# Optimization experiments

Hardware: AMD Instinct MI355X
Metric: run time of the kernel (lower is better)

The kernel has to match this reference:

```python
import jax, jax.numpy as jnp
import numpy as np

WS = 16                     # window_size
OW = 24                     # overlap_win_size = int(16*0.5)+16
PAD = (OW - WS) // 2        # unfold padding = 4
DIM = 384
HEADS = 6
HID = 768                   # mlp_ratio 2.0 * dim
TABLE = (WS + OW - 1) ** 2  # 1521


def _rel_pos_index():
    ch = np.arange(WS)
    coords = np.stack(np.meshgrid(ch, ch, indexing='ij')).reshape(2, -1)      # (2, WS*WS)
    co = np.arange(OW)
    coords_o = np.stack(np.meshgrid(co, co, indexing='ij')).reshape(2, -1)    # (2, OW*OW)
    rel = coords[:, :, None] - coords_o[:, None, :]                           # (2, nq, nk)
    rel = rel.transpose(1, 2, 0).astype(np.int64)
    rel[..., 0] += OW - 1
    rel[..., 1] += OW - 1
    rel[..., 0] *= WS + OW - 1
    return rel.sum(-1)                                                        # (WS*WS, OW*OW)

RPI = jnp.asarray(_rel_pos_index())


def _ln(x, g, b, eps=1e-5):
    m = x.mean(-1, keepdims=True)
    v = ((x - m) ** 2).mean(-1, keepdims=True)
    return (x - m) / jnp.sqrt(v + eps) * g + b


def _overlap_windows(t, H, W):
    # t: (B,H,W,C) -> (B*nw, OW*OW, C); overlapping patches, stride WS, pad PAD
    B, _, _, C = t.shape
    nH, nW = H // WS, W // WS
    tp = jnp.pad(t, ((0, 0), (PAD, PAD), (PAD, PAD), (0, 0)))
    r = (jnp.arange(nH) * WS)[:, None] + jnp.arange(OW)   # (nH, OW)
    c = (jnp.arange(nW) * WS)[:, None] + jnp.arange(OW)   # (nW, OW)
    p = tp[:, r]              # (B, nH, OW, Wp, C)
    p = p[:, :, :, c]         # (B, nH, OW, nW, OW, C)
    p = p.transpose(0, 1, 3, 2, 4, 5).reshape(B * nH * nW, OW * OW, C)
    return p


def setup_inputs() -> dict:
    key = jax.random.key(0)
    ks = jax.random.split(key, 8)
    H = W = 192
    B = 1
    inp = {
        'x': jax.random.normal(ks[0], (B, H * W, DIM), dtype=jnp.float32),
        'norm1_g': jnp.ones((DIM,), jnp.float32),
        'norm1_b': jnp.zeros((DIM,), jnp.float32),
        'qkv_w': jax.random.normal(ks[1], (DIM, 3 * DIM), jnp.float32) * 0.02,
        'qkv_b': jnp.zeros((3 * DIM,), jnp.float32),
        'rpb_table': jax.random.normal(ks[2], (TABLE, HEADS), jnp.float32) * 0.02,
        'proj_w': jax.random.normal(ks[3], (DIM, DIM), jnp.float32) * 0.02,
        'proj_b': jnp.zeros((DIM,), jnp.float32),
        'norm2_g': jnp.ones((DIM,), jnp.float32),
        'norm2_b': jnp.zeros((DIM,), jnp.float32),
        'fc1_w': jax.random.normal(ks[4], (DIM, HID), jnp.float32) * 0.02,
        'fc1_b': jnp.zeros((HID,), jnp.float32),
        'fc2_w': jax.random.normal(ks[5], (HID, DIM), jnp.float32) * 0.02,
        'fc2_b': jnp.zeros((DIM,), jnp.float32),
        'H': H,
        'W': W,
    }
    return inp


def reference(x, norm1_g, norm1_b, qkv_w, qkv_b, rpb_table, proj_w, proj_b,
              norm2_g, norm2_b, fc1_w, fc1_b, fc2_w, fc2_b, H, W):
    B, L, C = x.shape
    d = C // HEADS
    scale = d ** (-0.5)
    nH, nW = H // WS, W // WS

    shortcut = x
    xn = _ln(x, norm1_g, norm1_b).reshape(B, H, W, C)
    qkv = xn @ qkv_w + qkv_b                                   # (B,H,W,3C)
    q, k, v = qkv[..., :C], qkv[..., C:2 * C], qkv[..., 2 * C:]

    # non-overlapping query windows: (B*nw, WS*WS, C)
    qw = q.reshape(B, nH, WS, nW, WS, C).transpose(0, 1, 3, 2, 4, 5).reshape(-1, WS * WS, C)
    # overlapping key/value windows: (B*nw, OW*OW, C)
    kw = _overlap_windows(k, H, W)
    vw = _overlap_windows(v, H, W)

    b_ = qw.shape[0]
    qh = qw.reshape(b_, WS * WS, HEADS, d) * scale
    kh = kw.reshape(b_, OW * OW, HEADS, d)
    vh = vw.reshape(b_, OW * OW, HEADS, d)

    attn = jnp.einsum('bqhd,bkhd->bhqk', qh, kh)               # (b_, H, nq, nk)
    bias = rpb_table[RPI].transpose(2, 0, 1)                   # (heads, nq, nk)
    attn = jax.nn.softmax(attn + bias[None], axis=-1)
    out = jnp.einsum('bhqk,bkhd->bqhd', attn, vh).reshape(b_, WS * WS, C)

    # window reverse -> (B, H*W, C)
    out = out.reshape(B, nH, nW, WS, WS, C).transpose(0, 1, 3, 2, 4, 5).reshape(B, H * W, C)
    out = out @ proj_w + proj_b

    x = shortcut + out
    h = _ln(x, norm2_g, norm2_b)
    h = jax.nn.gelu(h @ fc1_w + fc1_b, approximate=False)
    h = h @ fc2_w + fc2_b
    return x + h
```

## Files before the change

### kernel.cpp

```cpp
#include <hip/hip_runtime.h>

#define LTOK 36864
#define DIMC 384
#define NHEADS 6
#define HDIM 64
#define HIDD 768
#define NWIN 12
#define WSZ 16
#define OWS 24
#define KVTOK 576

using bf16x8 = __attribute__((ext_vector_type(8))) short;
using f32x4  = __attribute__((ext_vector_type(4))) float;

__device__ inline unsigned short f2bf(float f) {
  unsigned u = __float_as_uint(f);
  return (unsigned short)((u + 0x7FFFu + ((u >> 16) & 1u)) >> 16);
}
__device__ __forceinline__ unsigned cvt_pk_bf16(float lo, float hi) {
  unsigned r;
  asm volatile("v_cvt_pk_bf16_f32 %0, %1, %2" : "=v"(r) : "v"(lo), "v"(hi));
  return r;
}
__device__ __forceinline__ unsigned short f2bf1(float x) {
  return (unsigned short)(cvt_pk_bf16(x, x) & 0xffffu);
}
__device__ __forceinline__ float fexp2(float x) {
#if __has_builtin(__builtin_amdgcn_exp2f)
  return __builtin_amdgcn_exp2f(x);
#else
  return exp2f(x);
#endif
}

typedef __attribute__((address_space(1))) const unsigned int GAS_U32;
typedef __attribute__((address_space(3))) unsigned int LAS_U32;
__device__ __forceinline__ void gl16(const void* g, void* l) {
  __builtin_amdgcn_global_load_lds((GAS_U32*)g, (LAS_U32*)l, 16, 0, 0);
}

__global__ void prep_kernel(const float* __restrict__ qkv_w, const float* __restrict__ proj_w,
                            const float* __restrict__ fc1_w, const float* __restrict__ fc2_w,
                            unsigned short* __restrict__ wq, unsigned short* __restrict__ wp,
                            unsigned short* __restrict__ w1, unsigned short* __restrict__ w2) {
  int id = blockIdx.x * 256 + threadIdx.x;
  if (id < 442368) {
    int n = id / 384, k = id - n * 384;
    wq[id] = f2bf(qkv_w[(size_t)k * 1152 + n]);
  } else if (id < 589824) {
    int i = id - 442368;
    int n = i / 384, k = i - n * 384;
    wp[i] = f2bf(proj_w[(size_t)k * 384 + n]);
  } else if (id < 884736) {
    int i = id - 589824;
    int n = i / 384, k = i - n * 384;
    w1[i] = f2bf(fc1_w[(size_t)k * 768 + n]);
  } else {
    int i = id - 884736;
    int n = i / 768, k = i - n * 768;
    w2[i] = f2bf(fc2_w[(size_t)k * 384 + n]);
  }
}

__global__ void rpb_expand_kernel(const float* __restrict__ rpb, float* __restrict__ biasm8) {
  int id = blockIdx.x * 256 + threadIdx.x;
  if (id >= NHEADS * 256 * 576) return;
  int head = id / 147456;
  int rem = id - head * 147456;
  int q = rem / 576;
  int kt = rem - q * 576;
  int ty = q >> 4, tx = q & 15;
  int oy = kt / 24, ox = kt - (kt / 24) * 24;
  biasm8[id] = rpb[((ty - oy + 23) * 39 + (tx - ox + 23)) * NHEADS + head] * 8.0f;
}

__global__ __launch_bounds__(256) void ln_kernel(const float* __restrict__ x,
                                                 const float* __restrict__ g,
                                                 const float* __restrict__ b,
                                                 unsigned short* __restrict__ out) {
  int row = blockIdx.x * 4 + (threadIdx.x >> 6);
  int lane = threadIdx.x & 63;
  const float* xr = x + (size_t)row * DIMC;
  float v[6];
  float s = 0.f, ss = 0.f;
#pragma unroll
  for (int i = 0; i < 6; ++i) {
    v[i] = xr[lane + i * 64];
    s += v[i];
    ss += v[i] * v[i];
  }
#pragma unroll
  for (int off = 32; off; off >>= 1) {
    s += __shfl_xor(s, off);
    ss += __shfl_xor(ss, off);
  }
  float mean = s * (1.f / DIMC);
  float var = ss * (1.f / DIMC) - mean * mean;
  float rstd = rsqrtf(var + 1e-5f);
  unsigned short* outr = out + (size_t)row * DIMC;
#pragma unroll
  for (int i = 0; i < 6; ++i) {
    int c = lane + i * 64;
    outr[c] = f2bf((v[i] - mean) * rstd * g[c] + b[c]);
  }
}

template <int EPI>
__global__ __launch_bounds__(256) void gemm_bf16(const unsigned short* __restrict__ A,
                                                 const unsigned short* __restrict__ Bt,
                                                 const float* __restrict__ bias,
                                                 const float* __restrict__ resid,
                                                 void* __restrict__ outv,
                                                 int M, int N, int K) {
  __shared__ unsigned short As[3][4096];
  __shared__ unsigned short Bs[3][4096];
  const int tid = threadIdx.x;
  int id = blockIdx.y * gridDim.x + blockIdx.x;
  int chunk = (gridDim.x * gridDim.y) >> 3;
  int lid = (id & 7) * chunk + (id >> 3);
  const int m0 = (lid / gridDim.x) * 128;
  const int n0 = (lid % gridDim.x) * 128;
  const int lane = tid & 63;
  const int wave = tid >> 6;
  const int wr = wave >> 1;
  const int wc = wave & 1;
  const int l15 = lane & 15, l4 = lane >> 4;

  f32x4 acc[4][4];
#pragma unroll
  for (int i = 0; i < 4; ++i)
#pragma unroll
    for (int j = 0; j < 4; ++j) acc[i][j] = (f32x4){0.f, 0.f, 0.f, 0.f};

  const int srow = tid >> 2;
  const int scol = (tid & 3) << 3;
  const unsigned short* ga = A + (size_t)(m0 + srow) * K + scol;
  const unsigned short* gb = Bt + (size_t)(n0 + srow) * K + scol;

#define STAGE(buf, k0)                                        \
  do {                                                        \
    unsigned short* lA = As[buf] + wave * 512;                \
    unsigned short* lB = Bs[buf] + wave * 512;                \
    gl16(ga + (k0), lA);                                      \
    gl16(ga + (size_t)64 * K + (k0), lA + 2048);              \
    gl16(gb + (k0), lB);                                      \
    gl16(gb + (size_t)64 * K + (k0), lB + 2048);              \
  } while (0)

  const int nt = K >> 5;
  STAGE(0, 0);
  STAGE(1, 32);

  for (int t = 0; t < nt; ++t) {
    const int cur = t % 3;
    asm volatile("s_waitcnt vmcnt(4)" ::: "memory");
    __builtin_amdgcn_s_barrier();

    if (t + 2 < nt) STAGE((t + 2) % 3, (t + 2) * 32);

    const unsigned short* arp = As[cur] + (wr * 64 + l15) * 32 + l4 * 8;
    const unsigned short* brp = Bs[cur] + (wc * 64 + l15) * 32 + l4 * 8;
    bf16x8 af[4], bfr[4];
#pragma unroll
    for (int i = 0; i < 4; ++i) af[i] = *(const bf16x8*)(arp + i * 512);
#pragma unroll
    for (int j = 0; j < 4; ++j) bfr[j] = *(const bf16x8*)(brp + j * 512);
#pragma unroll
    for (int i = 0; i < 4; ++i)
#pragma unroll
      for (int j = 0; j < 4; ++j)
        acc[i][j] = __builtin_amdgcn_mfma_f32_16x16x32_bf16(af[i], bfr[j], acc[i][j], 0, 0, 0);
  }
#undef STAGE
  asm volatile("s_waitcnt vmcnt(0)" ::: "memory");

#pragma unroll
  for (int j = 0; j < 4; ++j) {
    int gcol = n0 + wc * 64 + j * 16 + l15;
    float bv = bias[gcol];
#pragma unroll
    for (int i = 0; i < 4; ++i) {
#pragma unroll
      for (int r = 0; r < 4; ++r) {
        int grow = m0 + wr * 64 + i * 16 + l4 * 4 + r;
        float v = acc[i][j][r] + bv;
        size_t idx = (size_t)grow * N + gcol;
        if (EPI == 0) {
          ((unsigned short*)outv)[idx] = f2bf(v);
        } else if (EPI == 1) {
          ((float*)outv)[idx] = resid[idx] + v;
        } else {
          float gv = 0.5f * v * (1.f + erff(v * 0.70710678118654752f));
          ((unsigned short*)outv)[idx] = f2bf(gv);
        }
      }
    }
  }
}

__global__ __launch_bounds__(256, 3) void attn_kernel(const unsigned short* __restrict__ qkv,
                                                      const float* __restrict__ biasm8,
                                                      unsigned short* __restrict__ att) {
  __shared__ unsigned short ks[2][64][72];
  __shared__ unsigned short vts[2][64][72];
  __shared__ unsigned short pt[4][32][40];
  int bid = blockIdx.x;
  int lid = (bid & 7) * 216 + (bid >> 3);
  const int hw = lid >> 1;
  const int qh = lid & 1;
  const int win = hw / NHEADS;
  const int head = hw - win * NHEADS;
  const int wy = win / NWIN, wx = win - (win / NWIN) * NWIN;
  const int tid = threadIdx.x;
  const int w = tid >> 6, lane = tid & 63;
  const int l15 = lane & 15, l4 = lane >> 4;
  const float SC02 = 0.125f * 1.44269504f;
  const float C0 = -8.f * 1.44269504f;

  const int qrow0 = qh * 128 + w * 32;

  bf16x8 qf[2][2];
#pragma unroll
  for (int jq = 0; jq < 2; ++jq) {
    int q = qrow0 + jq * 16 + l15;
    int gy = wy * WSZ + (q >> 4), gx = wx * WSZ + (q & 15);
    const unsigned short* qp = qkv + (size_t)(gy * 192 + gx) * 1152 + head * HDIM + l4 * 8;
    qf[jq][0] = *(const bf16x8*)qp;
    qf[jq][1] = *(const bf16x8*)(qp + 32);
  }

  const float* bias_base = biasm8 + (size_t)head * 147456 + (size_t)(qrow0 + l15) * 576 + l4 * 4;

#define KS_W(buf, k0v, k1v)                          \
  do {                                               \
    *(uint4*)&ks[buf][lane][w * 16] = (k0v);         \
    *(uint4*)&ks[buf][lane][w * 16 + 8] = (k1v);     \
  } while (0)
#define VTS_W(buf, v0v, v1v)                                           \
  do {                                                                 \
    const unsigned short* vv = (const unsigned short*)&(v0v);          \
    _Pragma("unroll") for (int j = 0; j < 8; ++j)                      \
        vts[buf][w * 16 + j][lane] = vv[j];                            \
    vv = (const unsigned short*)&(v1v);                                \
    _Pragma("unroll") for (int j = 0; j < 8; ++j)                      \
        vts[buf][w * 16 + 8 + j][lane] = vv[j];                        \
  } while (0)

  {
    int kt = lane;
    int oy = kt / OWS, ox = kt - (kt / OWS) * OWS;
    int gy = wy * WSZ + oy - 4, gx = wx * WSZ + ox - 4;
    uint4 k0 = {0,0,0,0}, k1 = {0,0,0,0}, v0 = {0,0,0,0}, v1 = {0,0,0,0};
    if ((unsigned)gy < 192u && (unsigned)gx < 192u) {
      const unsigned short* gp = qkv + (size_t)(gy * 192 + gx) * 1152 + DIMC + head * HDIM + w * 16;
      k0 = *(const uint4*)gp;         k1 = *(const uint4*)(gp + 8);
      v0 = *(const uint4*)(gp + 384); v1 = *(const uint4*)(gp + 392);
    }
    KS_W(0, k0, k1);
    VTS_W(0, v0, v1);
  }

  f32x4 sacc[4][2];
#pragma unroll
  for (int i = 0; i < 4; ++i)
#pragma unroll
    for (int j2 = 0; j2 < 2; ++j2)
      sacc[i][j2] = *(const f32x4*)(bias_base + j2 * (16 * 576) + i * 16);

  __syncthreads();

  f32x4 oacc[2][4];
#pragma unroll
  for (int i = 0; i < 2; ++i)
#pragma unroll
    for (int j = 0; j < 4; ++j) oacc[i][j] = (f32x4){0.f, 0.f, 0.f, 0.f};
  float plsum[2] = {0.f, 0.f};

  for (int kb = 0; kb < 9; ++kb) {
    const int cur = kb & 1;
    const bool have = kb < 8;
    uint4 pk0 = {0,0,0,0}, pk1 = {0,0,0,0}, pv0 = {0,0,0,0}, pv1 = {0,0,0,0};
    if (have) {
      int kt = (kb + 1) * 64 + lane;
      int oy = kt / OWS, ox = kt - (kt / OWS) * OWS;
      int gy = wy * WSZ + oy - 4, gx = wx * WSZ + ox - 4;
      if ((unsigned)gy < 192u && (unsigned)gx < 192u) {
        const unsigned short* gp = qkv + (size_t)(gy * 192 + gx) * 1152 + DIMC + head * HDIM + w * 16;
        pk0 = *(const uint4*)gp;         pk1 = *(const uint4*)(gp + 8);
        pv0 = *(const uint4*)(gp + 384); pv1 = *(const uint4*)(gp + 392);
      }
    }

#pragma unroll
    for (int kk = 0; kk < 2; ++kk) {
      bf16x8 kf[4];
#pragma unroll
      for (int i = 0; i < 4; ++i)
        kf[i] = *(const bf16x8*)&ks[cur][i * 16 + l15][kk * 32 + l4 * 8];
      __builtin_amdgcn_s_setprio(1);
#pragma unroll
      for (int i = 0; i < 4; ++i)
#pragma unroll
        for (int j2 = 0; j2 < 2; ++j2)
          sacc[i][j2] = __builtin_amdgcn_mfma_f32_16x16x32_bf16(kf[i], qf[j2][kk], sacc[i][j2], 0, 0, 0);
      __builtin_amdgcn_s_setprio(0);
    }

#pragma unroll
    for (int i = 0; i < 4; ++i)
#pragma unroll
      for (int j2 = 0; j2 < 2; ++j2)
#pragma unroll
        for (int r = 0; r < 4; ++r) {
          float p = fexp2(fmaf(sacc[i][j2][r], SC02, C0));
          sacc[i][j2][r] = p;
          plsum[j2] += p;
        }

#pragma unroll
    for (int kk = 0; kk < 2; ++kk) {
#pragma unroll
      for (int i2 = 0; i2 < 2; ++i2)
#pragma unroll
        for (int j2 = 0; j2 < 2; ++j2) {
          int i = kk * 2 + i2;
          uint2 pk;
          pk.x = cvt_pk_bf16(sacc[i][j2][0], sacc[i][j2][1]);
          pk.y = cvt_pk_bf16(sacc[i][j2][2], sacc[i][j2][3]);
          *(uint2*)&pt[w][j2 * 16 + l15][i2 * 16 + l4 * 4] = pk;
        }
      bf16x8 pf[2], vf[4];
#pragma unroll
      for (int j2 = 0; j2 < 2; ++j2)
        pf[j2] = *(const bf16x8*)&pt[w][j2 * 16 + l15][l4 * 8];
#pragma unroll
      for (int jd = 0; jd < 4; ++jd)
        vf[jd] = *(const bf16x8*)&vts[cur][jd * 16 + l15][kk * 32 + l4 * 8];
      __builtin_amdgcn_s_setprio(1);
#pragma unroll
      for (int j2 = 0; j2 < 2; ++j2)
#pragma unroll
        for (int jd = 0; jd < 4; ++jd)
          oacc[j2][jd] = __builtin_amdgcn_mfma_f32_16x16x32_bf16(pf[j2], vf[jd], oacc[j2][jd], 0, 0, 0);
      __builtin_amdgcn_s_setprio(0);
    }

    if (have) {
      KS_W(cur ^ 1, pk0, pk1);
      VTS_W(cur ^ 1, pv0, pv1);
      const float* bp = bias_base + (kb + 1) * 64;
#pragma unroll
      for (int i = 0; i < 4; ++i)
#pragma unroll
        for (int j2 = 0; j2 < 2; ++j2)
          sacc[i][j2] = *(const f32x4*)(bp + j2 * (16 * 576) + i * 16);
    }
    __syncthreads();
  }
#undef KS_W
#undef VTS_W

  float invl[2];
#pragma unroll
  for (int j2 = 0; j2 < 2; ++j2) {
    plsum[j2] += __shfl_xor(plsum[j2], 16);
    plsum[j2] += __shfl_xor(plsum[j2], 32);
    invl[j2] = 1.f / plsum[j2];
  }

#pragma unroll
  for (int j2 = 0; j2 < 2; ++j2) {
#pragma unroll
    for (int r = 0; r < 4; ++r) {
      float il = __shfl(invl[j2], l4 * 4 + r);
      int q = qrow0 + j2 * 16 + l4 * 4 + r;
      int gy = wy * WSZ + (q >> 4), gx = wx * WSZ + (q & 15);
      unsigned short* op = att + (size_t)(gy * 192 + gx) * DIMC + head * HDIM + l15;
#pragma unroll
      for (int jd = 0; jd < 4; ++jd) op[jd * 16] = f2bf1(oacc[j2][jd][r] * il);
    }
  }
}

extern "C" void kernel_launch(void* const* d_in, const int* in_sizes, int n_in,
                              void* d_out, int out_size, void* d_ws, size_t ws_size,
                              hipStream_t stream) {
  const float* x      = (const float*)d_in[0];
  const float* n1g    = (const float*)d_in[1];
  const float* n1b    = (const float*)d_in[2];
  const float* qkv_w  = (const float*)d_in[3];
  const float* qkv_b  = (const float*)d_in[4];
  const float* rpb    = (const float*)d_in[5];
  const float* proj_w = (const float*)d_in[6];
  const float* proj_b = (const float*)d_in[7];
  const float* n2g    = (const float*)d_in[8];
  const float* n2b    = (const float*)d_in[9];
  const float* fc1_w  = (const float*)d_in[10];
  const float* fc1_b  = (const float*)d_in[11];
  const float* fc2_w  = (const float*)d_in[12];
  const float* fc2_b  = (const float*)d_in[13];
  float* out = (float*)d_out;

  char* ws = (char*)d_ws;
  unsigned short* xn   = (unsigned short*)ws;
  unsigned short* qkvb = (unsigned short*)(ws + 28311552);
  unsigned short* att  = (unsigned short*)(ws + 28311552 + 84934656);
  unsigned short* wq   = (unsigned short*)(ws + 141557760);
  unsigned short* wp   = wq + 1152 * 384;
  unsigned short* w1   = wp + 384 * 384;
  unsigned short* w2   = w1 + 768 * 384;
  float* biasm8 = (float*)ws;

  prep_kernel<<<4608, 256, 0, stream>>>(qkv_w, proj_w, fc1_w, fc2_w, wq, wp, w1, w2);

  ln_kernel<<<LTOK / 4, 256, 0, stream>>>(x, n1g, n1b, xn);
  gemm_bf16<0><<<dim3(1152 / 128, LTOK / 128), 256, 0, stream>>>(xn, wq, qkv_b, nullptr, qkvb,
                                                                 LTOK, 1152, DIMC);
  rpb_expand_kernel<<<(NHEADS * 256 * 576 + 255) / 256, 256, 0, stream>>>(rpb, biasm8);
  attn_kernel<<<dim3(NHEADS * 144 * 2), 256, 0, stream>>>(qkvb, biasm8, att);
  gemm_bf16<1><<<dim3(DIMC / 128, LTOK / 128), 256, 0, stream>>>(att, wp, proj_b, x, out,
                                                                 LTOK, DIMC, DIMC);
  ln_kernel<<<LTOK / 4, 256, 0, stream>>>(out, n2g, n2b, xn);
  gemm_bf16<2><<<dim3(HIDD / 128, LTOK / 128), 256, 0, stream>>>(xn, w1, fc1_b, nullptr, qkvb,
                                                                 LTOK, HIDD, DIMC);
  gemm_bf16<1><<<dim3(DIMC / 128, LTOK / 128), 256, 0, stream>>>(qkvb, w2, fc2_b, out, out,
                                                                 LTOK, DIMC, HIDD);
}
```

Baseline: 330.9 us.

## Load GEMM B fragments directly from global and prefetch attention bias earlier

In the bf16 GEMM, the B operand no longer goes through shared memory. Each wave loads its own B fragments straight from global memory into registers every k-step, and the vmcnt wait thresholds are adjusted to match. This removes half the LDS staging traffic, but B is now read redundantly across waves and its load latency is exposed inside the loop. In the attention kernel, the next block's relative-position bias is prefetched into a separate register set between the two QK MFMA halves, so the load overlaps with compute at the cost of more registers.

```diff
diff --git a/kernel.cpp b/kernel.cpp
--- a/kernel.cpp
+++ b/kernel.cpp
@@ -113,7 +113,6 @@
                                                  void* __restrict__ outv,
                                                  int M, int N, int K) {
   __shared__ unsigned short As[3][4096];
-  __shared__ unsigned short Bs[3][4096];
   const int tid = threadIdx.x;
   int id = blockIdx.y * gridDim.x + blockIdx.x;
   int chunk = (gridDim.x * gridDim.y) >> 3;
@@ -135,16 +134,13 @@
   const int srow = tid >> 2;
   const int scol = (tid & 3) << 3;
   const unsigned short* ga = A + (size_t)(m0 + srow) * K + scol;
-  const unsigned short* gb = Bt + (size_t)(n0 + srow) * K + scol;
+  const unsigned short* gB = Bt + (size_t)(n0 + wc * 64 + l15) * K + l4 * 8;
 
 #define STAGE(buf, k0)                                        \
   do {                                                        \
     unsigned short* lA = As[buf] + wave * 512;                \
-    unsigned short* lB = Bs[buf] + wave * 512;                \
     gl16(ga + (k0), lA);                                      \
     gl16(ga + (size_t)64 * K + (k0), lA + 2048);              \
-    gl16(gb + (k0), lB);                                      \
-    gl16(gb + (size_t)64 * K + (k0), lB + 2048);              \
   } while (0)
 
   const int nt = K >> 5;
@@ -153,18 +149,24 @@
 
   for (int t = 0; t < nt; ++t) {
     const int cur = t % 3;
-    asm volatile("s_waitcnt vmcnt(4)" ::: "memory");
+    bf16x8 bfr[4];
+#pragma unroll
+    for (int j = 0; j < 4; ++j)
+      bfr[j] = *(const bf16x8*)(gB + (size_t)(j * 16) * K + t * 32);
+
+    if (t + 1 < nt) {
+      asm volatile("s_waitcnt vmcnt(6)" ::: "memory");
+    } else {
+      asm volatile("s_waitcnt vmcnt(4)" ::: "memory");
+    }
     __builtin_amdgcn_s_barrier();
 
     if (t + 2 < nt) STAGE((t + 2) % 3, (t + 2) * 32);
 
     const unsigned short* arp = As[cur] + (wr * 64 + l15) * 32 + l4 * 8;
-    const unsigned short* brp = Bs[cur] + (wc * 64 + l15) * 32 + l4 * 8;
-    bf16x8 af[4], bfr[4];
+    bf16x8 af[4];
 #pragma unroll
     for (int i = 0; i < 4; ++i) af[i] = *(const bf16x8*)(arp + i * 512);
-#pragma unroll
-    for (int j = 0; j < 4; ++j) bfr[j] = *(const bf16x8*)(brp + j * 512);
 #pragma unroll
     for (int i = 0; i < 4; ++i)
 #pragma unroll
@@ -260,12 +262,12 @@
     VTS_W(0, v0, v1);
   }
 
-  f32x4 sacc[4][2];
+  f32x4 bnext[4][2];
 #pragma unroll
   for (int i = 0; i < 4; ++i)
 #pragma unroll
     for (int j2 = 0; j2 < 2; ++j2)
-      sacc[i][j2] = *(const f32x4*)(bias_base + j2 * (16 * 576) + i * 16);
+      bnext[i][j2] = *(const f32x4*)(bias_base + j2 * (16 * 576) + i * 16);
 
   __syncthreads();
 
@@ -291,18 +293,39 @@
       }
     }
 
-#pragma unroll
-    for (int kk = 0; kk < 2; ++kk) {
+    f32x4 sacc[4][2];
+    {
       bf16x8 kf[4];
 #pragma unroll
       for (int i = 0; i < 4; ++i)
-        kf[i] = *(const bf16x8*)&ks[cur][i * 16 + l15][kk * 32 + l4 * 8];
+        kf[i] = *(const bf16x8*)&ks[cur][i * 16 + l15][l4 * 8];
       __builtin_amdgcn_s_setprio(1);
 #pragma unroll
       for (int i = 0; i < 4; ++i)
 #pragma unroll
         for (int j2 = 0; j2 < 2; ++j2)
-          sacc[i][j2] = __builtin_amdgcn_mfma_f32_16x16x32_bf16(kf[i], qf[j2][kk], sacc[i][j2], 0, 0, 0);
+          sacc[i][j2] = __builtin_amdgcn_mfma_f32_16x16x32_bf16(kf[i], qf[j2][0], bnext[i][j2], 0, 0, 0);
+      __builtin_amdgcn_s_setprio(0);
+    }
+    if (have) {
+      const float* bp = bias_base + (kb + 1) * 64;
+#pragma unroll
+      for (int i = 0; i < 4; ++i)
+#pragma unroll
+        for (int j2 = 0; j2 < 2; ++j2)
+          bnext[i][j2] = *(const f32x4*)(bp + j2 * (16 * 576) + i * 16);
+    }
+    {
+      bf16x8 kf[4];
+#pragma unroll
+      for (int i = 0; i < 4; ++i)
+        kf[i] = *(const bf16x8*)&ks[cur][i * 16 + l15][32 + l4 * 8];
+      __builtin_amdgcn_s_setprio(1);
+#pragma unroll
+      for (int i = 0; i < 4; ++i)
+#pragma unroll
+        for (int j2 = 0; j2 < 2; ++j2)
+          sacc[i][j2] = __builtin_amdgcn_mfma_f32_16x16x32_bf16(kf[i], qf[j2][1], sacc[i][j2], 0, 0, 0);
       __builtin_amdgcn_s_setprio(0);
     }
 
@@ -348,12 +371,6 @@
     if (have) {
       KS_W(cur ^ 1, pk0, pk1);
       VTS_W(cur ^ 1, pv0, pv1);
-      const float* bp = bias_base + (kb + 1) * 64;
-#pragma unroll
-      for (int i = 0; i < 4; ++i)
-#pragma unroll
-        for (int j2 = 0; j2 < 2; ++j2)
-          sacc[i][j2] = *(const f32x4*)(bp + j2 * (16 * 576) + i * 16);
     }
     __syncthreads();
   }
```

Result: slower. 401.4 us (+21.3%).

## Store intermediate residual in bf16 and compute softmax row sums with MFMA

Applied to the files above, without the earlier changes.

The residual after the projection GEMM is now written as bf16 into a separate buffer instead of fp32 into the output. The second LayerNorm and the fc2 epilogue read that bf16 copy, which cuts memory traffic for the intermediate activation but adds bf16 rounding to the residual path. In attention, the per-row softmax denominator is now accumulated by an extra MFMA against a vector of ones, replacing the scalar sums and cross-lane shuffles. The GEMM loop also waits for all loads on its last iteration, so the trailing wait after the loop is gone.

```diff
diff --git a/kernel.cpp b/kernel.cpp
--- a/kernel.cpp
+++ b/kernel.cpp
@@ -16,6 +16,9 @@
 __device__ inline unsigned short f2bf(float f) {
   unsigned u = __float_as_uint(f);
   return (unsigned short)((u + 0x7FFFu + ((u >> 16) & 1u)) >> 16);
+}
+__device__ inline float bf2f(unsigned short h) {
+  return __uint_as_float(((unsigned)h) << 16);
 }
 __device__ __forceinline__ unsigned cvt_pk_bf16(float lo, float hi) {
   unsigned r;
@@ -74,18 +77,20 @@
   biasm8[id] = rpb[((ty - oy + 23) * 39 + (tx - ox + 23)) * NHEADS + head] * 8.0f;
 }
 
-__global__ __launch_bounds__(256) void ln_kernel(const float* __restrict__ x,
+template <int BF16IN>
+__global__ __launch_bounds__(256) void ln_kernel(const void* __restrict__ xv,
                                                  const float* __restrict__ g,
                                                  const float* __restrict__ b,
                                                  unsigned short* __restrict__ out) {
   int row = blockIdx.x * 4 + (threadIdx.x >> 6);
   int lane = threadIdx.x & 63;
-  const float* xr = x + (size_t)row * DIMC;
   float v[6];
   float s = 0.f, ss = 0.f;
 #pragma unroll
   for (int i = 0; i < 6; ++i) {
-    v[i] = xr[lane + i * 64];
+    int c = lane + i * 64;
+    if (BF16IN) v[i] = bf2f(((const unsigned short*)xv)[(size_t)row * DIMC + c]);
+    else        v[i] = ((const float*)xv)[(size_t)row * DIMC + c];
     s += v[i];
     ss += v[i] * v[i];
   }
@@ -109,7 +114,7 @@
 __global__ __launch_bounds__(256) void gemm_bf16(const unsigned short* __restrict__ A,
                                                  const unsigned short* __restrict__ Bt,
                                                  const float* __restrict__ bias,
-                                                 const float* __restrict__ resid,
+                                                 const void* __restrict__ residv,
                                                  void* __restrict__ outv,
                                                  int M, int N, int K) {
   __shared__ unsigned short As[3][4096];
@@ -153,7 +158,11 @@
 
   for (int t = 0; t < nt; ++t) {
     const int cur = t % 3;
-    asm volatile("s_waitcnt vmcnt(4)" ::: "memory");
+    if (t + 1 < nt) {
+      asm volatile("s_waitcnt vmcnt(4)" ::: "memory");
+    } else {
+      asm volatile("s_waitcnt vmcnt(0)" ::: "memory");
+    }
     __builtin_amdgcn_s_barrier();
 
     if (t + 2 < nt) STAGE((t + 2) % 3, (t + 2) * 32);
@@ -172,7 +181,6 @@
         acc[i][j] = __builtin_amdgcn_mfma_f32_16x16x32_bf16(af[i], bfr[j], acc[i][j], 0, 0, 0);
   }
 #undef STAGE
-  asm volatile("s_waitcnt vmcnt(0)" ::: "memory");
 
 #pragma unroll
   for (int j = 0; j < 4; ++j) {
@@ -187,11 +195,13 @@
         size_t idx = (size_t)grow * N + gcol;
         if (EPI == 0) {
           ((unsigned short*)outv)[idx] = f2bf(v);
-        } else if (EPI == 1) {
-          ((float*)outv)[idx] = resid[idx] + v;
-        } else {
+        } else if (EPI == 2) {
           float gv = 0.5f * v * (1.f + erff(v * 0.70710678118654752f));
           ((unsigned short*)outv)[idx] = f2bf(gv);
+        } else if (EPI == 3) {
+          ((unsigned short*)outv)[idx] = f2bf(((const float*)residv)[idx] + v);
+        } else {
+          ((float*)outv)[idx] = bf2f(((const unsigned short*)residv)[idx]) + v;
         }
       }
     }
@@ -216,6 +226,8 @@
   const int l15 = lane & 15, l4 = lane >> 4;
   const float SC02 = 0.125f * 1.44269504f;
   const float C0 = -8.f * 1.44269504f;
+  const bf16x8 ones = {(short)0x3F80, (short)0x3F80, (short)0x3F80, (short)0x3F80,
+                       (short)0x3F80, (short)0x3F80, (short)0x3F80, (short)0x3F80};
 
   const int qrow0 = qh * 128 + w * 32;
 
@@ -274,7 +286,9 @@
   for (int i = 0; i < 2; ++i)
 #pragma unroll
     for (int j = 0; j < 4; ++j) oacc[i][j] = (f32x4){0.f, 0.f, 0.f, 0.f};
-  float plsum[2] = {0.f, 0.f};
+  f32x4 ol[2];
+  ol[0] = (f32x4){0.f, 0.f, 0.f, 0.f};
+  ol[1] = (f32x4){0.f, 0.f, 0.f, 0.f};
 
   for (int kb = 0; kb < 9; ++kb) {
     const int cur = kb & 1;
@@ -311,11 +325,8 @@
 #pragma unroll
       for (int j2 = 0; j2 < 2; ++j2)
 #pragma unroll
-        for (int r = 0; r < 4; ++r) {
-          float p = fexp2(fmaf(sacc[i][j2][r], SC02, C0));
-          sacc[i][j2][r] = p;
-          plsum[j2] += p;
-        }
+        for (int r = 0; r < 4; ++r)
+          sacc[i][j2][r] = fexp2(fmaf(sacc[i][j2][r], SC02, C0));
 
 #pragma unroll
     for (int kk = 0; kk < 2; ++kk) {
@@ -338,10 +349,12 @@
         vf[jd] = *(const bf16x8*)&vts[cur][jd * 16 + l15][kk * 32 + l4 * 8];
       __builtin_amdgcn_s_setprio(1);
 #pragma unroll
-      for (int j2 = 0; j2 < 2; ++j2)
+      for (int j2 = 0; j2 < 2; ++j2) {
 #pragma unroll
         for (int jd = 0; jd < 4; ++jd)
           oacc[j2][jd] = __builtin_amdgcn_mfma_f32_16x16x32_bf16(pf[j2], vf[jd], oacc[j2][jd], 0, 0, 0);
+        ol[j2] = __builtin_amdgcn_mfma_f32_16x16x32_bf16(pf[j2], ones, ol[j2], 0, 0, 0);
+      }
       __builtin_amdgcn_s_setprio(0);
     }
 
@@ -360,19 +373,11 @@
 #undef KS_W
 #undef VTS_W
 
-  float invl[2];
 #pragma unroll
   for (int j2 = 0; j2 < 2; ++j2) {
-    plsum[j2] += __shfl_xor(plsum[j2], 16);
-    plsum[j2] += __shfl_xor(plsum[j2], 32);
-    invl[j2] = 1.f / plsum[j2];
-  }
-
-#pragma unroll
-  for (int j2 = 0; j2 < 2; ++j2) {
 #pragma unroll
     for (int r = 0; r < 4; ++r) {
-      float il = __shfl(invl[j2], l4 * 4 + r);
+      float il = 1.f / ol[j2][r];
       int q = qrow0 + j2 * 16 + l4 * 4 + r;
       int gy = wy * WSZ + (q >> 4), gx = wx * WSZ + (q & 15);
       unsigned short* op = att + (size_t)(gy * 192 + gx) * DIMC + head * HDIM + l15;
@@ -404,6 +409,7 @@
   char* ws = (char*)d_ws;
   unsigned short* xn   = (unsigned short*)ws;
   unsigned short* qkvb = (unsigned short*)(ws + 28311552);
+  unsigned short* xa   = (unsigned short*)(ws + 28311552 + 56623104);
   unsigned short* att  = (unsigned short*)(ws + 28311552 + 84934656);
   unsigned short* wq   = (unsigned short*)(ws + 141557760);
   unsigned short* wp   = wq + 1152 * 384;
@@ -413,16 +419,16 @@
 
   prep_kernel<<<4608, 256, 0, stream>>>(qkv_w, proj_w, fc1_w, fc2_w, wq, wp, w1, w2);
 
-  ln_kernel<<<LTOK / 4, 256, 0, stream>>>(x, n1g, n1b, xn);
+  ln_kernel<0><<<LTOK / 4, 256, 0, stream>>>(x, n1g, n1b, xn);
   gemm_bf16<0><<<dim3(1152 / 128, LTOK / 128), 256, 0, stream>>>(xn, wq, qkv_b, nullptr, qkvb,
                                                                  LTOK, 1152, DIMC);
   rpb_expand_kernel<<<(NHEADS * 256 * 576 + 255) / 256, 256, 0, stream>>>(rpb, biasm8);
   attn_kernel<<<dim3(NHEADS * 144 * 2), 256, 0, stream>>>(qkvb, biasm8, att);
-  gemm_bf16<1><<<dim3(DIMC / 128, LTOK / 128), 256, 0, stream>>>(att, wp, proj_b, x, out,
+  gemm_bf16<3><<<dim3(DIMC / 128, LTOK / 128), 256, 0, stream>>>(att, wp, proj_b, x, xa,
                                                                  LTOK, DIMC, DIMC);
-  ln_kernel<<<LTOK / 4, 256, 0, stream>>>(out, n2g, n2b, xn);
+  ln_kernel<1><<<LTOK / 4, 256, 0, stream>>>(xa, n2g, n2b, xn);
   gemm_bf16<2><<<dim3(HIDD / 128, LTOK / 128), 256, 0, stream>>>(xn, w1, fc1_b, nullptr, qkvb,
                                                                  LTOK, HIDD, DIMC);
-  gemm_bf16<1><<<dim3(DIMC / 128, LTOK / 128), 256, 0, stream>>>(qkvb, w2, fc2_b, out, out,
+  gemm_bf16<4><<<dim3(DIMC / 128, LTOK / 128), 256, 0, stream>>>(qkvb, w2, fc2_b, xa, out,
                                                                  LTOK, DIMC, HIDD);
 }
```

Result: faster. 317.6 us (-4.0%).
